# Kernel optimization log

Hardware: AMD Instinct MI355X
Metric: run time of the kernel (lower is better)

## Reference

```python
import jax, jax.numpy as jnp
import numpy as np

EPS = 1e-5  # torch LayerNorm default

def _ln(x, g, b):
    m = jnp.mean(x, axis=-1, keepdims=True)
    v = jnp.mean((x - m) ** 2, axis=-1, keepdims=True)
    return (x - m) * jax.lax.rsqrt(v + EPS) * g + b

def setup_inputs() -> dict:
    key = jax.random.key(0)
    ks = jax.random.split(key, 12)
    N_sup = N_res = 768
    c_z = 128   # input_dim
    c = 128     # num_intermediate_channel
    c_out = 128 # output_dim
    s = 0.02
    d = {}
    d["act_s"] = jax.random.normal(ks[0], (N_sup, N_sup, c_z), jnp.float32)
    d["act_r"] = jax.random.normal(ks[1], (N_res, N_res, c_z), jnp.float32)
    d["mask_r"] = (jax.random.uniform(ks[2], (N_res, N_res)) > 0.1).astype(jnp.float32)
    # input LayerNorm params
    d["ln_in_g"] = jnp.ones((c_z,), jnp.float32)
    d["ln_in_b"] = jnp.zeros((c_z,), jnp.float32)
    # projections (stored as [in, out], y = x @ W + b)
    d["w_lp"] = (jax.random.normal(ks[3], (c_z, c)) * s).astype(jnp.float32)
    d["b_lp"] = jnp.zeros((c,), jnp.float32)
    d["w_rp"] = (jax.random.normal(ks[4], (c_z, c)) * s).astype(jnp.float32)
    d["b_rp"] = jnp.zeros((c,), jnp.float32)
    # gates (bias_init=1)
    d["w_lg"] = (jax.random.normal(ks[5], (c_z, c)) * s).astype(jnp.float32)
    d["b_lg"] = jnp.ones((c,), jnp.float32)
    d["w_rg"] = (jax.random.normal(ks[6], (c_z, c)) * s).astype(jnp.float32)
    d["b_rg"] = jnp.ones((c,), jnp.float32)
    # center LayerNorm
    d["ln_c_g"] = jnp.ones((c,), jnp.float32)
    d["ln_c_b"] = jnp.zeros((c,), jnp.float32)
    # output projection
    d["w_out"] = (jax.random.normal(ks[7], (c, c_out)) * s).astype(jnp.float32)
    d["b_out"] = jnp.zeros((c_out,), jnp.float32)
    return d

def reference(act_s, act_r, mask_r, ln_in_g, ln_in_b, w_lp, b_lp, w_rp, b_rp,
              w_lg, b_lg, w_rg, b_rg, ln_c_g, ln_c_b, w_out, b_out):
    m = mask_r[..., None]                                   # [N_res, N_res, 1]
    s = _ln(act_s, ln_in_g, ln_in_b)                        # [N_sup, N_sup, c_z]
    r = _ln(act_r, ln_in_g, ln_in_b)                        # [N_res, N_res, c_z]
    left = (s @ w_lp + b_lp) * jax.nn.sigmoid(s @ w_lg + b_lg)
    right = (m * (r @ w_rp + b_rp)) * jax.nn.sigmoid(r @ w_rg + b_rg)
    left_line = left.sum(axis=0)                            # [N_sup, c] (aggr_by_row)
    right_line = right.sum(axis=0)                          # [N_res, c]
    act = jnp.einsum('ik,jk->ijk', left_line, right_line)   # [N_sup, N_res, c]
    act = _ln(act, ln_c_g, ln_c_b)
    return act @ w_out + b_out                              # [N_sup, N_res, c_out]
```

## Files before the change

### kernel.cpp

```cpp
#include <hip/hip_runtime.h>
#include <math.h>

#define NRES 768
#define C    128
#define LNEPS 1e-5f
#define TA   16
#define ACH  48
#define MI   16
#define NIT  (NRES / MI)
#define XBUF (MI * 256)
#define LHALF (ACH * NIT)
#define OSC  0.015625f

typedef __attribute__((ext_vector_type(8))) _Float16 f16x8;
typedef __attribute__((ext_vector_type(4))) float   f32x4;

__device__ __forceinline__ uint32_t pk_f16rn(float a, float b) {
    _Float16 ha = (_Float16)a, hb = (_Float16)b;
    const uint32_t ua = *(const unsigned short*)&ha;
    const uint32_t ub = *(const unsigned short*)&hb;
    return ua | (ub << 16);
}

__device__ __forceinline__ void stage_row2(const float4& x, int row, int t,
                                           char* hiB, char* sqB) {
    const int byte = (row * 256 + 8 * (t & 31)) ^ ((row & 15) << 4);
    uint2 uh, uq;
    uh.x = pk_f16rn(x.x, x.y);
    uh.y = pk_f16rn(x.z, x.w);
    uq.x = pk_f16rn(x.x * x.x, x.y * x.y);
    uq.y = pk_f16rn(x.z * x.z, x.w * x.w);
    *(uint2*)(hiB + byte) = uh;
    *(uint2*)(sqB + byte) = uq;
}

__global__ __launch_bounds__(256, 3) void line_all(
    const float* __restrict__ act_s, const float* __restrict__ act_r,
    const float* __restrict__ mask,
    const float* __restrict__ ln_g, const float* __restrict__ ln_b,
    const float* __restrict__ w_lp, const float* __restrict__ b_lp,
    const float* __restrict__ w_rp, const float* __restrict__ b_rp,
    const float* __restrict__ w_lg, const float* __restrict__ b_lg,
    const float* __restrict__ w_rg, const float* __restrict__ b_rg,
    float* __restrict__ part)
{
    __shared__ char  sHi[XBUF];
    __shared__ char  sSq[XBUF];
    __shared__ float sM[TA * MI];

    const int t = threadIdx.x;
    const int w = t >> 6;
    const int l = t & 63;
    const int right = (blockIdx.x >= LHALF);
    const int bid2  = blockIdx.x - right * LHALF;
    const int i0  = (bid2 % NIT) * MI;
    const int ach = bid2 / NIT;
    const int a0  = ach * TA;

    const float* act = right ? act_r : act_s;
    const float* wP  = right ? w_rp : w_lp;
    const float* bP  = right ? b_rp : b_lp;
    const float* wG  = right ? w_rg : w_lg;
    const float* bG  = right ? b_rg : b_lg;

    f16x8 bfr[4][4];
    float sQ[4], cB[4];
#pragma unroll
    for (int nt = 0; nt < 4; ++nt) {
        const float* wsrc = (nt < 2) ? wP : wG;
        const int n = w * 32 + (nt & 1) * 16 + (l & 15);
        float sacc = 0.f, tacc = 0.f;
#pragma unroll
        for (int kk = 0; kk < 4; ++kk) {
            f16x8 f;
#pragma unroll
            for (int jj = 0; jj < 8; ++jj) {
                const int k = kk * 32 + (l >> 4) * 8 + jj;
                const float wv = wsrc[k * C + n];
                const _Float16 q = (_Float16)(ln_g[k] * wv);
                f[jj] = q;
                sacc += (float)q;
                tacc += ln_b[k] * wv;
            }
            bfr[nt][kk] = f;
        }
        sacc += __shfl_xor(sacc, 16); sacc += __shfl_xor(sacc, 32);
        tacc += __shfl_xor(tacc, 16); tacc += __shfl_xor(tacc, 32);
        sQ[nt] = sacc;
        cB[nt] = tacc + ((nt < 2) ? bP[n] : bG[n]);
    }

    f16x8 onesf;
#pragma unroll
    for (int jj = 0; jj < 8; ++jj) onesf[jj] = (_Float16)1.0f;

    if (right) {
        sM[t] = mask[(size_t)(a0 + (t >> 4)) * NRES + i0 + (t & 15)];
    }

    float lacc[2][4];
#pragma unroll
    for (int ntp = 0; ntp < 2; ++ntp)
#pragma unroll
        for (int jr = 0; jr < 4; ++jr) lacc[ntp][jr] = 0.f;

    const float* srcbase = act + (size_t)a0 * (NRES * C) + (size_t)i0 * C;

    float4 xv[2], xn[2];
#pragma unroll
    for (int j = 0; j < 2; ++j)
        xv[j] = *(const float4*)(srcbase + 4 * (t + 256 * j));

    for (int al = 0; al < TA; ++al) {
        if (al + 1 < TA) {
            const float* srcn = srcbase + (size_t)(al + 1) * (NRES * C);
#pragma unroll
            for (int j = 0; j < 2; ++j)
                xn[j] = *(const float4*)(srcn + 4 * (t + 256 * j));
        }

#pragma unroll
        for (int j = 0; j < 2; ++j)
            stage_row2(xv[j], (t >> 5) + 8 * j, t, sHi, sSq);
        __syncthreads();

        const f32x4 zero = {0.f, 0.f, 0.f, 0.f};
        f32x4 acc[4], accS = zero, accS2 = zero;
#pragma unroll
        for (int nt = 0; nt < 4; ++nt) acc[nt] = zero;

#pragma unroll
        for (int kk = 0; kk < 4; ++kk) {
            const int row  = l & 15;
            const int byte = (row * 256 + (kk * 32 + (l >> 4) * 8) * 2) ^ ((row & 15) << 4);
            const f16x8 ah  = *(const f16x8*)(sHi + byte);
            const f16x8 asq = *(const f16x8*)(sSq + byte);
            acc[0] = __builtin_amdgcn_mfma_f32_16x16x32_f16(ah,  bfr[0][kk], acc[0], 0, 0, 0);
            acc[1] = __builtin_amdgcn_mfma_f32_16x16x32_f16(ah,  bfr[1][kk], acc[1], 0, 0, 0);
            acc[2] = __builtin_amdgcn_mfma_f32_16x16x32_f16(ah,  bfr[2][kk], acc[2], 0, 0, 0);
            acc[3] = __builtin_amdgcn_mfma_f32_16x16x32_f16(ah,  bfr[3][kk], acc[3], 0, 0, 0);
            accS   = __builtin_amdgcn_mfma_f32_16x16x32_f16(ah,  onesf, accS,  0, 0, 0);
            accS2  = __builtin_amdgcn_mfma_f32_16x16x32_f16(asq, onesf, accS2, 0, 0, 0);
        }

        float mk[4] = {1.f, 1.f, 1.f, 1.f};
        if (right) {
            const float4 m4 = *(const float4*)&sM[al * MI + (l >> 4) * 4];
            mk[0] = m4.x; mk[1] = m4.y; mk[2] = m4.z; mk[3] = m4.w;
        }
#pragma unroll
        for (int jr = 0; jr < 4; ++jr) {
            const float m_  = accS[jr] * (1.f / C);
            const float var = accS2[jr] * (1.f / C) - m_ * m_;
            const float inv = rsqrtf(var + LNEPS);
#pragma unroll
            for (int ntp = 0; ntp < 2; ++ntp) {
                const float P = (acc[ntp][jr]     - m_ * sQ[ntp])     * inv + cB[ntp];
                const float G = (acc[ntp + 2][jr] - m_ * sQ[ntp + 2]) * inv + cB[ntp + 2];
                const float sg = __builtin_amdgcn_rcpf(1.f + __expf(-G));
                lacc[ntp][jr] += P * sg * mk[jr];
            }
        }
        __syncthreads();

        xv[0] = xn[0]; xv[1] = xn[1];
    }

    float* dst = part + ((size_t)right * ACH + ach) * (NRES * C);
#pragma unroll
    for (int ntp = 0; ntp < 2; ++ntp)
#pragma unroll
        for (int jr = 0; jr < 4; ++jr)
            dst[(size_t)(i0 + (l >> 4) * 4 + jr) * C +
                w * 32 + ntp * 16 + (l & 15)] = lacc[ntp][jr];
}

__global__ __launch_bounds__(256) void reduce2(const float* __restrict__ part,
                                               float* __restrict__ left_line,
                                               float* __restrict__ right_line) {
    const int half = (blockIdx.x >= 384);
    const int idx  = (blockIdx.x - half * 384) * 256 + threadIdx.x;
    const float* p = part + (size_t)half * ACH * NRES * C;
    float s = 0.f;
#pragma unroll 8
    for (int q = 0; q < ACH; ++q) s += p[(size_t)q * (NRES * C) + idx];
    (half ? right_line : left_line)[idx] = s;
}

__global__ __launch_bounds__(256, 3) void out_mfma(
    const float* __restrict__ lline,
    const float* __restrict__ rline,
    const float* __restrict__ cg, const float* __restrict__ cb,
    const float* __restrict__ wO, const float* __restrict__ bO,
    float* __restrict__ out)
{
    __shared__ char sHi[64 * 256];
    __shared__ char sSq[64 * 256];

    const int t = threadIdx.x;
    const int w = t >> 6;
    const int l = t & 63;
    const int i = blockIdx.x;

    f16x8 bfr[2][4];
    float sQ[2], cB[2];
#pragma unroll
    for (int nt = 0; nt < 2; ++nt) {
        const int n = w * 32 + nt * 16 + (l & 15);
        float sacc = 0.f, tacc = 0.f;
#pragma unroll
        for (int kk = 0; kk < 4; ++kk) {
            f16x8 f;
#pragma unroll
            for (int jj = 0; jj < 8; ++jj) {
                const int k = kk * 32 + (l >> 4) * 8 + jj;
                const float wv = wO[k * C + n];
                const _Float16 q = (_Float16)(cg[k] * wv);
                f[jj] = q;
                sacc += (float)q;
                tacc += cb[k] * wv;
            }
            bfr[nt][kk] = f;
        }
        sacc += __shfl_xor(sacc, 16); sacc += __shfl_xor(sacc, 32);
        tacc += __shfl_xor(tacc, 16); tacc += __shfl_xor(tacc, 32);
        sQ[nt] = sacc;
        cB[nt] = tacc + bO[n];
    }

    f16x8 onesf;
#pragma unroll
    for (int jj = 0; jj < 8; ++jj) onesf[jj] = (_Float16)1.0f;

    const int c4 = 4 * (t & 31);
    float4 l4 = *(const float4*)(lline + (size_t)i * C + c4);
    l4.x *= OSC; l4.y *= OSC; l4.z *= OSC; l4.w *= OSC;

    for (int jt = 0; jt < 12; ++jt) {
        const int j0 = jt * 64;
        const float* rsrc = rline + (size_t)j0 * C;

        float4 rv[8];
#pragma unroll
        for (int j = 0; j < 8; ++j)
            rv[j] = *(const float4*)(rsrc + 4 * (t + 256 * j));
#pragma unroll
        for (int j = 0; j < 8; ++j) {
            float4 p;
            p.x = l4.x * rv[j].x; p.y = l4.y * rv[j].y;
            p.z = l4.z * rv[j].z; p.w = l4.w * rv[j].w;
            stage_row2(p, (t >> 5) + 8 * j, t, sHi, sSq);
        }
        __syncthreads();

        const f32x4 zero = {0.f, 0.f, 0.f, 0.f};
#pragma unroll
        for (int mt = 0; mt < 4; ++mt) {
            f32x4 acc[2], accS = zero, accS2 = zero;
#pragma unroll
            for (int nt = 0; nt < 2; ++nt) acc[nt] = zero;
#pragma unroll
            for (int kk = 0; kk < 4; ++kk) {
                const int row  = mt * 16 + (l & 15);
                const int byte = (row * 256 + (kk * 32 + (l >> 4) * 8) * 2) ^ ((row & 15) << 4);
                const f16x8 ah  = *(const f16x8*)(sHi + byte);
                const f16x8 asq = *(const f16x8*)(sSq + byte);
                acc[0] = __builtin_amdgcn_mfma_f32_16x16x32_f16(ah,  bfr[0][kk], acc[0], 0, 0, 0);
                acc[1] = __builtin_amdgcn_mfma_f32_16x16x32_f16(ah,  bfr[1][kk], acc[1], 0, 0, 0);
                accS   = __builtin_amdgcn_mfma_f32_16x16x32_f16(ah,  onesf, accS,  0, 0, 0);
                accS2  = __builtin_amdgcn_mfma_f32_16x16x32_f16(asq, onesf, accS2, 0, 0, 0);
            }
#pragma unroll
            for (int jr = 0; jr < 4; ++jr) {
                const float m_  = accS[jr] * (1.f / C);
                const float var = accS2[jr] * (1.f / C) - m_ * m_;
                const float inv = rsqrtf(var + LNEPS * OSC * OSC);
#pragma unroll
                for (int nt = 0; nt < 2; ++nt)
                    out[((size_t)i * NRES + j0 + mt * 16 + (l >> 4) * 4 + jr) * C +
                        w * 32 + nt * 16 + (l & 15)] =
                        (acc[nt][jr] - m_ * sQ[nt]) * inv + cB[nt];
            }
        }
        __syncthreads();
    }
}

extern "C" void kernel_launch(void* const* d_in, const int* in_sizes, int n_in,
                              void* d_out, int out_size, void* d_ws, size_t ws_size,
                              hipStream_t stream) {
    const float* act_s = (const float*)d_in[0];
    const float* act_r = (const float*)d_in[1];
    const float* mask  = (const float*)d_in[2];
    const float* ln_g  = (const float*)d_in[3];
    const float* ln_b  = (const float*)d_in[4];
    const float* w_lp  = (const float*)d_in[5];
    const float* b_lp  = (const float*)d_in[6];
    const float* w_rp  = (const float*)d_in[7];
    const float* b_rp  = (const float*)d_in[8];
    const float* w_lg  = (const float*)d_in[9];
    const float* b_lg  = (const float*)d_in[10];
    const float* w_rg  = (const float*)d_in[11];
    const float* b_rg  = (const float*)d_in[12];
    const float* ln_cg = (const float*)d_in[13];
    const float* ln_cb = (const float*)d_in[14];
    const float* w_out = (const float*)d_in[15];
    const float* b_out = (const float*)d_in[16];
    float* out = (float*)d_out;

    float* part       = (float*)d_ws;
    float* left_line  = part + (size_t)2 * ACH * NRES * C;
    float* right_line = left_line + NRES * C;

    line_all<<<2 * LHALF, 256, 0, stream>>>(act_s, act_r, mask, ln_g, ln_b,
                                            w_lp, b_lp, w_rp, b_rp,
                                            w_lg, b_lg, w_rg, b_rg, part);
    reduce2<<<768, 256, 0, stream>>>(part, left_line, right_line);
    out_mfma<<<NRES, 256, 0, stream>>>(left_line, right_line, ln_cg, ln_cb,
                                       w_out, b_out, out);
}
```

Measured before the change: 360.3 us.

## Stage activation tiles via async global-to-LDS loads with double buffering

Replaces the register prefetch plus f16/square staging into two LDS arrays with direct `global_load_lds` DMA of raw fp32 rows into double-buffered LDS. The global addresses are swizzled so the linear LDS layout matches a conflict-free read pattern. Each wave now reads fp32 from LDS and converts to f16 and squared f16 at MFMA-operand time, and one barrier per iteration is dropped. The aim is to overlap HBM loads with compute and cut VGPR staging and barriers. In exchange, all four waves repeat the conversion for the shared A tile, and correctness depends on the barrier waiting for the DMA to complete.

```diff
diff --git a/kernel.cpp b/kernel.cpp
--- a/kernel.cpp
+++ b/kernel.cpp
@@ -8,9 +8,12 @@
 #define ACH  48
 #define MI   16
 #define NIT  (NRES / MI)
-#define XBUF (MI * 256)
 #define LHALF (ACH * NIT)
+#define ASTRIDE (NRES * C * 4)
 #define OSC  0.015625f
+
+#define AS1 __attribute__((address_space(1)))
+#define AS3 __attribute__((address_space(3)))
 
 typedef __attribute__((ext_vector_type(8))) _Float16 f16x8;
 typedef __attribute__((ext_vector_type(4))) float   f32x4;
@@ -44,8 +47,8 @@
     const float* __restrict__ w_rg, const float* __restrict__ b_rg,
     float* __restrict__ part)
 {
-    __shared__ char  sHi[XBUF];
-    __shared__ char  sSq[XBUF];
+    __shared__ __align__(16) char sA[8192];
+    __shared__ __align__(16) char sB[8192];
     __shared__ float sM[TA * MI];
 
     const int t = threadIdx.x;
@@ -104,25 +107,36 @@
 #pragma unroll
         for (int jr = 0; jr < 4; ++jr) lacc[ntp][jr] = 0.f;
 
-    const float* srcbase = act + (size_t)a0 * (NRES * C) + (size_t)i0 * C;
-
-    float4 xv[2], xn[2];
-#pragma unroll
-    for (int j = 0; j < 2; ++j)
-        xv[j] = *(const float4*)(srcbase + 4 * (t + 256 * j));
+    const char* srcbase = (const char*)(act + (size_t)a0 * (NRES * C) + (size_t)i0 * C);
+
+    const int lin0 = w * 2048 + l * 16;
+    const int lin1 = lin0 + 1024;
+    const int sw0  = lin0 ^ (((lin0 >> 9) & 7) << 4);
+    const int sw1  = lin1 ^ (((lin1 >> 9) & 7) << 4);
+    const char* gq0 = srcbase + sw0;
+    const char* gq1 = srcbase + sw1;
+
+    __builtin_amdgcn_global_load_lds((const AS1 uint32_t*)gq0,
+                                     (AS3 uint32_t*)(sA + w * 2048), 16, 0, 0);
+    __builtin_amdgcn_global_load_lds((const AS1 uint32_t*)gq1,
+                                     (AS3 uint32_t*)(sA + w * 2048 + 1024), 16, 0, 0);
+    gq0 += ASTRIDE; gq1 += ASTRIDE;
+    __syncthreads();
+
+    const int r  = l & 15;
+    const int rx = l & 7;
 
     for (int al = 0; al < TA; ++al) {
+        const char* cur = (al & 1) ? sB : sA;
+        char*       nxt = (al & 1) ? sA : sB;
+
         if (al + 1 < TA) {
-            const float* srcn = srcbase + (size_t)(al + 1) * (NRES * C);
-#pragma unroll
-            for (int j = 0; j < 2; ++j)
-                xn[j] = *(const float4*)(srcn + 4 * (t + 256 * j));
-        }
-
-#pragma unroll
-        for (int j = 0; j < 2; ++j)
-            stage_row2(xv[j], (t >> 5) + 8 * j, t, sHi, sSq);
-        __syncthreads();
+            __builtin_amdgcn_global_load_lds((const AS1 uint32_t*)gq0,
+                                             (AS3 uint32_t*)(nxt + w * 2048), 16, 0, 0);
+            __builtin_amdgcn_global_load_lds((const AS1 uint32_t*)gq1,
+                                             (AS3 uint32_t*)(nxt + w * 2048 + 1024), 16, 0, 0);
+            gq0 += ASTRIDE; gq1 += ASTRIDE;
+        }
 
         const f32x4 zero = {0.f, 0.f, 0.f, 0.f};
         f32x4 acc[4], accS = zero, accS2 = zero;
@@ -131,16 +145,28 @@
 
 #pragma unroll
         for (int kk = 0; kk < 4; ++kk) {
-            const int row  = l & 15;
-            const int byte = (row * 256 + (kk * 32 + (l >> 4) * 8) * 2) ^ ((row & 15) << 4);
-            const f16x8 ah  = *(const f16x8*)(sHi + byte);
-            const f16x8 asq = *(const f16x8*)(sSq + byte);
-            acc[0] = __builtin_amdgcn_mfma_f32_16x16x32_f16(ah,  bfr[0][kk], acc[0], 0, 0, 0);
-            acc[1] = __builtin_amdgcn_mfma_f32_16x16x32_f16(ah,  bfr[1][kk], acc[1], 0, 0, 0);
-            acc[2] = __builtin_amdgcn_mfma_f32_16x16x32_f16(ah,  bfr[2][kk], acc[2], 0, 0, 0);
-            acc[3] = __builtin_amdgcn_mfma_f32_16x16x32_f16(ah,  bfr[3][kk], acc[3], 0, 0, 0);
-            accS   = __builtin_amdgcn_mfma_f32_16x16x32_f16(ah,  onesf, accS,  0, 0, 0);
-            accS2  = __builtin_amdgcn_mfma_f32_16x16x32_f16(asq, onesf, accS2, 0, 0, 0);
+            const int ch0 = kk * 8 + (l >> 4) * 2;
+            const int ad0 = r * 512 + (((ch0)     ^ rx) << 4);
+            const int ad1 = r * 512 + (((ch0 + 1) ^ rx) << 4);
+            const float4 xa = *(const float4*)(cur + ad0);
+            const float4 xb = *(const float4*)(cur + ad1);
+
+            f16x8 xf, qf;
+            xf[0] = (_Float16)xa.x; xf[1] = (_Float16)xa.y;
+            xf[2] = (_Float16)xa.z; xf[3] = (_Float16)xa.w;
+            xf[4] = (_Float16)xb.x; xf[5] = (_Float16)xb.y;
+            xf[6] = (_Float16)xb.z; xf[7] = (_Float16)xb.w;
+            qf[0] = (_Float16)(xa.x * xa.x); qf[1] = (_Float16)(xa.y * xa.y);
+            qf[2] = (_Float16)(xa.z * xa.z); qf[3] = (_Float16)(xa.w * xa.w);
+            qf[4] = (_Float16)(xb.x * xb.x); qf[5] = (_Float16)(xb.y * xb.y);
+            qf[6] = (_Float16)(xb.z * xb.z); qf[7] = (_Float16)(xb.w * xb.w);
+
+            acc[0] = __builtin_amdgcn_mfma_f32_16x16x32_f16(xf, bfr[0][kk], acc[0], 0, 0, 0);
+            acc[1] = __builtin_amdgcn_mfma_f32_16x16x32_f16(xf, bfr[1][kk], acc[1], 0, 0, 0);
+            acc[2] = __builtin_amdgcn_mfma_f32_16x16x32_f16(xf, bfr[2][kk], acc[2], 0, 0, 0);
+            acc[3] = __builtin_amdgcn_mfma_f32_16x16x32_f16(xf, bfr[3][kk], acc[3], 0, 0, 0);
+            accS   = __builtin_amdgcn_mfma_f32_16x16x32_f16(xf, onesf, accS,  0, 0, 0);
+            accS2  = __builtin_amdgcn_mfma_f32_16x16x32_f16(qf, onesf, accS2, 0, 0, 0);
         }
 
         float mk[4] = {1.f, 1.f, 1.f, 1.f};
@@ -161,9 +187,8 @@
                 lacc[ntp][jr] += P * sg * mk[jr];
             }
         }
+
         __syncthreads();
-
-        xv[0] = xn[0]; xv[1] = xn[1];
     }
 
     float* dst = part + ((size_t)right * ACH + ach) * (NRES * C);
```

After: 391.2 us. 1.09x slower.
